# Performance work log

Measured on AMD Instinct MI355X. Metric: run time of the kernel, lower is better.

Reference implementation:

```python
import jax, jax.numpy as jnp
import numpy as np

SIGMA = 0.248
PRNUM = 6
P = 7.5
K = 3.0
ALPHA = 2.5


def _gauss_kernel():
    # 5x5 normalized Gaussian, replicated per channel for depthwise conv [O=3,I=1,5,5]
    x = jnp.arange(-2, 3, dtype=jnp.float32)
    x2, y2 = jnp.meshgrid(x, x, indexing='xy')
    k = jnp.exp(-(x2 ** 2 + y2 ** 2) / (2.0 * SIGMA ** 2))
    k = k / jnp.sum(k)
    return jnp.broadcast_to(k[None, None], (3, 1, 5, 5))


def _dwconv(x, k):
    # x: [3,H,W]; depthwise 5x5 conv, padding=2 (matches F.conv2d(..., padding=2, groups=3))
    return jax.lax.conv_general_dilated(
        x[None], k, window_strides=(1, 1), padding=[(2, 2), (2, 2)],
        feature_group_count=3, dimension_numbers=('NCHW', 'OIHW', 'NCHW'))[0]


def _down2(x):
    # torch bilinear align_corners=False at exact scale 0.5 == 2x2 average pooling
    c, h, w = x.shape
    return x.reshape(c, h // 2, 2, w // 2, 2).mean(axis=(2, 4))


def _up(x, hw):
    # torch bilinear align_corners=False upsample (half-pixel centers) == jax linear resize
    return jax.image.resize(x, (x.shape[0], hw[0], hw[1]), method='linear')


def _foveate(img, fixs):
    C, H, W = img.shape
    k = _gauss_kernel()
    # build Gaussian pyramid
    G = img
    pyr = [G]
    for _ in range(1, PRNUM):
        G = _down2(_dwconv(G, k))
        pyr.append(G)
    # re-expand each level back to full res (interpolate then blur at each step)
    As = [pyr[0]]
    for i in range(1, PRNUM):
        cur = pyr[i]
        for j in range(i):
            hw = (cur.shape[1] * 2, cur.shape[2] * 2) if j < i - 1 else (H, W)
            cur = _dwconv(_up(cur, hw), k)
        As.append(cur)
    As = jnp.stack(As)  # [prNum, 3, H, W]

    # radial eccentricity map (min distance over fixations)
    x = jnp.arange(W, dtype=jnp.float32)
    y = jnp.arange(H, dtype=jnp.float32)
    x2d, y2d = jnp.meshgrid(x, y, indexing='xy')  # each [H, W]
    d = jnp.sqrt((x2d[None] - fixs[:, 0, None, None]) ** 2 +
                 (y2d[None] - fixs[:, 1, None, None]) ** 2) / P
    theta = jnp.min(d, axis=0)
    R = ALPHA / (theta + ALPHA)

    Ts = [jnp.exp(-((2.0 ** (i - 3)) * R / SIGMA) ** 2 * K) for i in range(1, PRNUM)]
    Ts.append(jnp.zeros_like(R))

    om = np.minimum(np.sqrt(np.log(2.0) / K) / (2.0 ** np.arange(-2, 3)) * SIGMA, 1.0)
    omega = np.concatenate([om, [0.0]]).astype(np.float32)  # [prNum]

    layer_ind = jnp.zeros_like(R)
    for i in range(1, PRNUM):
        ind = (R >= omega[i]) & (R <= omega[i - 1])
        layer_ind = jnp.where(ind, jnp.float32(i), layer_ind)

    Bs = [(0.5 - Ts[i]) / (Ts[i - 1] - Ts[i] + 1e-5) for i in range(1, PRNUM)]

    Ms = []
    for i in range(PRNUM):
        base = jnp.ones_like(R) if i == 0 else 1.0 - Bs[i - 1]
        M = jnp.where(layer_ind == i, base, jnp.float32(0.0))
        if i < PRNUM - 1:
            M = jnp.where(layer_ind == i + 1, Bs[i], M)
        Ms.append(M)
    Ms = jnp.stack(Ms)  # [prNum, H, W]

    # blend: sum_p Ms[p] * As[p, c]
    im_fov = jnp.einsum('phw,pchw->chw', Ms, As)
    return im_fov


def setup_inputs() -> dict:
    key = jax.random.key(0)
    k1, k2 = jax.random.split(key)
    img = jax.random.uniform(k1, (3, 2048, 2048), dtype=jnp.float32) * 255.0
    fixs = jax.random.uniform(k2, (4, 2), dtype=jnp.float32) * 2048.0
    return {'img': img, 'fixs': fixs}


def reference(img, fixs):
    return _foveate(img, fixs)
```

## Files before the change

kernel.cpp:

```cpp
#include <hip/hip_runtime.h>
#include <math.h>

#define HW2048 (2048ull*2048ull)
typedef float f4 __attribute__((ext_vector_type(4)));
typedef float f2 __attribute__((ext_vector_type(2)));

struct BP {
  float P[4][3];
  float D2[5];
  float cc[5];
};

__global__ __launch_bounds__(256) void down12_k(const float* __restrict__ img,
                                                float* __restrict__ C1,
                                                float* __restrict__ p2) {
  int X = blockIdx.x * 16 + threadIdx.x;
  int Y = blockIdx.y * 16 + threadIdx.y;
  int c = blockIdx.z;
  const float* ip = img + (size_t)c * HW2048 + (size_t)(4 * Y) * 2048 + 4 * X;
  f4 r0 = __builtin_nontemporal_load((const f4*)(ip));
  f4 r1 = __builtin_nontemporal_load((const f4*)(ip + 2048));
  f4 r2 = __builtin_nontemporal_load((const f4*)(ip + 4096));
  f4 r3 = __builtin_nontemporal_load((const f4*)(ip + 6144));
  float a00 = 0.25f * (r0.x + r0.y + r1.x + r1.y);
  float a01 = 0.25f * (r0.z + r0.w + r1.z + r1.w);
  float a10 = 0.25f * (r2.x + r2.y + r3.x + r3.y);
  float a11 = 0.25f * (r2.z + r2.w + r3.z + r3.w);
  float* cp = C1 + (size_t)c * 1048576 + (size_t)(2 * Y) * 1024 + 2 * X;
  f2 u; u.x = a00; u.y = a01; *(f2*)cp = u;
  f2 v; v.x = a10; v.y = a11; *(f2*)(cp + 1024) = v;
  p2[((size_t)c * 512 + Y) * 512 + X] = 0.25f * (a00 + a01 + a10 + a11);
}

__global__ __launch_bounds__(256) void down345_k(const float* __restrict__ p2,
                                                 float* __restrict__ p3,
                                                 float* __restrict__ p4,
                                                 float* __restrict__ p5) {
  __shared__ float t4[16][17];
  int tx = threadIdx.x, ty = threadIdx.y;
  int X = blockIdx.x * 16 + tx;
  int Y = blockIdx.y * 16 + ty;
  int c = blockIdx.z;
  const float* ip = p2 + (size_t)c * 262144 + (size_t)(4 * Y) * 512 + 4 * X;
  f4 r0 = *(const f4*)(ip);
  f4 r1 = *(const f4*)(ip + 512);
  f4 r2 = *(const f4*)(ip + 1024);
  f4 r3 = *(const f4*)(ip + 1536);
  float a00 = 0.25f * (r0.x + r0.y + r1.x + r1.y);
  float a01 = 0.25f * (r0.z + r0.w + r1.z + r1.w);
  float a10 = 0.25f * (r2.x + r2.y + r3.x + r3.y);
  float a11 = 0.25f * (r2.z + r2.w + r3.z + r3.w);
  float* cp = p3 + (size_t)c * 65536 + (size_t)(2 * Y) * 256 + 2 * X;
  f2 u; u.x = a00; u.y = a01; *(f2*)cp = u;
  f2 v; v.x = a10; v.y = a11; *(f2*)(cp + 256) = v;
  float m = 0.25f * (a00 + a01 + a10 + a11);
  t4[ty][tx] = m;
  p4[((size_t)c * 128 + Y) * 128 + X] = m;
  __syncthreads();
  int tid = ty * 16 + tx;
  if (tid < 64) {
    int y = tid >> 3, x = tid & 7;
    float w = 0.25f * (t4[2*y][2*x] + t4[2*y][2*x+1] + t4[2*y+1][2*x] + t4[2*y+1][2*x+1]);
    p5[((size_t)c * 64 + blockIdx.y * 8 + y) * 64 + blockIdx.x * 8 + x] = w;
  }
}

__device__ __forceinline__ void up_coords(int o, int n, int& i0, int& i1, float& w0) {
  int m = o >> 1;
  if (o & 1) { i0 = m; i1 = min(m + 1, n - 1); w0 = 0.75f; }
  else       { i0 = max(m - 1, 0); i1 = m;     w0 = 0.25f; }
}

__global__ __launch_bounds__(256) void upchain_k(const float* __restrict__ p3,
                                                 const float* __restrict__ p4,
                                                 const float* __restrict__ p5,
                                                 float* __restrict__ U3,
                                                 float* __restrict__ U4,
                                                 float* __restrict__ U5) {
  __shared__ float a[19][20];
  __shared__ float mid[34][35];
  int z = blockIdx.z, im = z / 3, ch = z - im * 3;
  int X0 = blockIdx.x * 64, Y0 = blockIdx.y * 64;
  int tid = threadIdx.x;
  int bx1 = X0 / 4 - 1, by1 = Y0 / 4 - 1;
  int bx2 = X0 / 2 - 1, by2 = Y0 / 2 - 1;

  if (im == 2) {
    const float* s = p5 + ch * 4096;
    for (int j = tid; j < 18 * 18; j += 256) {
      int r = j / 18, cc = j % 18;
      int gy = min(max(by1 + r, 0), 127), gx = min(max(bx1 + cc, 0), 127);
      int r0, r1, c0, c1; float wy0, wx0;
      up_coords(gy, 64, r0, r1, wy0);
      up_coords(gx, 64, c0, c1, wx0);
      float wy1 = 1.f - wy0, wx1 = 1.f - wx0;
      a[r][cc] = wy0 * (wx0 * s[r0*64+c0] + wx1 * s[r0*64+c1])
               + wy1 * (wx0 * s[r1*64+c0] + wx1 * s[r1*64+c1]);
    }
    __syncthreads();
    for (int j = tid; j < 34 * 34; j += 256) {
      int r = j / 34, cc = j % 34;
      int gy = min(max(by2 + r, 0), 255), gx = min(max(bx2 + cc, 0), 255);
      int r0, r1, c0, c1; float wy0, wx0;
      up_coords(gy, 128, r0, r1, wy0);
      up_coords(gx, 128, c0, c1, wx0);
      float wy1 = 1.f - wy0, wx1 = 1.f - wx0;
      int a0 = r0 - by1, a1 = r1 - by1, b0 = c0 - bx1, b1 = c1 - bx1;
      mid[r][cc] = wy0 * (wx0 * a[a0][b0] + wx1 * a[a0][b1])
                 + wy1 * (wx0 * a[a1][b0] + wx1 * a[a1][b1]);
    }
    __syncthreads();
  } else if (im == 1) {
    const float* s = p4 + ch * 16384;
    for (int j = tid; j < 34 * 34; j += 256) {
      int r = j / 34, cc = j % 34;
      int gy = min(max(by2 + r, 0), 255), gx = min(max(bx2 + cc, 0), 255);
      int r0, r1, c0, c1; float wy0, wx0;
      up_coords(gy, 128, r0, r1, wy0);
      up_coords(gx, 128, c0, c1, wx0);
      float wy1 = 1.f - wy0, wx1 = 1.f - wx0;
      mid[r][cc] = wy0 * (wx0 * s[r0*128+c0] + wx1 * s[r0*128+c1])
                 + wy1 * (wx0 * s[r1*128+c0] + wx1 * s[r1*128+c1]);
    }
    __syncthreads();
  }

  float* dst = (im == 0) ? U3 : (im == 1) ? U4 : U5;
  const float* p3g = p3 + ch * 65536;
  int lx = tid & 63, lyb = tid >> 6;
#pragma unroll 4
  for (int rr = 0; rr < 16; ++rr) {
    int ly = lyb * 16 + rr;
    int x = X0 + lx, y = Y0 + ly;
    int r0, r1, c0, c1; float wy0, wx0;
    up_coords(y, 256, r0, r1, wy0);
    up_coords(x, 256, c0, c1, wx0);
    float wy1 = 1.f - wy0, wx1 = 1.f - wx0;
    float v;
    if (im == 0) {
      v = wy0 * (wx0 * p3g[r0*256+c0] + wx1 * p3g[r0*256+c1])
        + wy1 * (wx0 * p3g[r1*256+c0] + wx1 * p3g[r1*256+c1]);
    } else {
      int a0 = r0 - by2, a1 = r1 - by2, b0 = c0 - bx2, b1 = c1 - bx2;
      v = wy0 * (wx0 * mid[a0][b0] + wx1 * mid[a0][b1])
        + wy1 * (wx0 * mid[a1][b0] + wx1 * mid[a1][b1]);
    }
    dst[((size_t)ch * 512 + y) * 512 + x] = v;
  }
}

__device__ __forceinline__ void s2c(const float* __restrict__ b, int x0, int y0,
                                    const BP& bp, float o[2][4]) {
  int t = x0 >> 2, ky = y0 >> 2, yph = y0 & 3;
  int c[3], r[3];
#pragma unroll
  for (int j = 0; j < 3; ++j) {
    c[j] = min(max(t - 1 + j, 0), 511);
    r[j] = min(max(ky - 1 + j, 0), 511);
  }
  float v[3][3];
#pragma unroll
  for (int j = 0; j < 3; ++j) {
    const float* row = b + r[j] * 512;
    v[j][0] = row[c[0]]; v[j][1] = row[c[1]]; v[j][2] = row[c[2]];
  }
  const float* wr0 = bp.P[yph];
  const float* wr1 = bp.P[yph + 1];
  float rv0[3], rv1[3];
#pragma unroll
  for (int i = 0; i < 3; ++i) {
    rv0[i] = wr0[0] * v[0][i] + wr0[1] * v[1][i] + wr0[2] * v[2][i];
    rv1[i] = wr1[0] * v[0][i] + wr1[1] * v[1][i] + wr1[2] * v[2][i];
  }
#pragma unroll
  for (int p = 0; p < 4; ++p) {
    o[0][p] = bp.P[p][0] * rv0[0] + bp.P[p][1] * rv0[1] + bp.P[p][2] * rv0[2];
    o[1][p] = bp.P[p][0] * rv1[0] + bp.P[p][1] * rv1[1] + bp.P[p][2] * rv1[2];
  }
}

__device__ __forceinline__ void s1c(const float* __restrict__ b, int x0, int y0,
                                    float o[2][4]) {
  int q0 = x0 >> 1, qy = y0 >> 1;
  int c[4], r[3];
#pragma unroll
  for (int i = 0; i < 4; ++i) c[i] = min(max(q0 - 1 + i, 0), 1023);
#pragma unroll
  for (int j = 0; j < 3; ++j) r[j] = min(max(qy - 1 + j, 0), 1023);
  float v[3][4];
#pragma unroll
  for (int j = 0; j < 3; ++j) {
    const float* row = b + r[j] * 1024;
    v[j][0] = row[c[0]]; v[j][1] = row[c[1]]; v[j][2] = row[c[2]]; v[j][3] = row[c[3]];
  }
  float rv0[4], rv1[4];
#pragma unroll
  for (int i = 0; i < 4; ++i) {
    rv0[i] = 0.25f * v[0][i] + 0.75f * v[1][i];
    rv1[i] = 0.75f * v[1][i] + 0.25f * v[2][i];
  }
  o[0][0] = 0.25f * rv0[0] + 0.75f * rv0[1];
  o[0][1] = 0.75f * rv0[1] + 0.25f * rv0[2];
  o[0][2] = 0.25f * rv0[1] + 0.75f * rv0[2];
  o[0][3] = 0.75f * rv0[2] + 0.25f * rv0[3];
  o[1][0] = 0.25f * rv1[0] + 0.75f * rv1[1];
  o[1][1] = 0.75f * rv1[1] + 0.25f * rv1[2];
  o[1][2] = 0.25f * rv1[1] + 0.75f * rv1[2];
  o[1][3] = 0.75f * rv1[2] + 0.25f * rv1[3];
}

__device__ __forceinline__ void sample_level(int l, int x0, int y0,
    const float* __restrict__ imgc, const float* __restrict__ C1c,
    const float* __restrict__ b2, const float* __restrict__ b3,
    const float* __restrict__ b4, const float* __restrict__ b5,
    const BP& bp, float o[2][4]) {
  if (l == 0) {
    f4 v0 = *(const f4*)(imgc + (size_t)y0 * 2048 + x0);
    f4 v1 = *(const f4*)(imgc + (size_t)(y0 + 1) * 2048 + x0);
    o[0][0] = v0.x; o[0][1] = v0.y; o[0][2] = v0.z; o[0][3] = v0.w;
    o[1][0] = v1.x; o[1][1] = v1.y; o[1][2] = v1.z; o[1][3] = v1.w;
  } else if (l == 1) {
    s1c(C1c, x0, y0, o);
  } else {
    const float* b = (l == 2) ? b2 : (l == 3) ? b3 : (l == 4) ? b4 : b5;
    s2c(b, x0, y0, bp, o);
  }
}

__global__ __launch_bounds__(256) void fblend_k(
    const float* __restrict__ img, const float* __restrict__ C1,
    const float* __restrict__ B2, const float* __restrict__ B3,
    const float* __restrict__ B4, const float* __restrict__ B5,
    const float* __restrict__ fixs, int nf,
    float* __restrict__ out, BP bp) {
  int xs = blockIdx.x * 64 + threadIdx.x;
  int yp = blockIdx.y * 4 + threadIdx.y;
  int x0 = xs * 4, y0 = yp * 2;
  size_t ob0 = (size_t)y0 * 2048 + x0;

  float d2[2][4];
#pragma unroll
  for (int j = 0; j < 2; ++j)
#pragma unroll
    for (int i = 0; i < 4; ++i) d2[j][i] = 3.4e38f;
  for (int f = 0; f < nf; ++f) {
    float dx0 = (float)x0 - fixs[2 * f], dy0 = (float)y0 - fixs[2 * f + 1];
#pragma unroll
    for (int j = 0; j < 2; ++j) {
      float dy = dy0 + (float)j, dy2 = dy * dy;
#pragma unroll
      for (int i = 0; i < 4; ++i) {
        float dx = dx0 + (float)i;
        d2[j][i] = fminf(d2[j][i], dx * dx + dy2);
      }
    }
  }

  float dmn = d2[0][0], dmx = d2[0][0];
#pragma unroll
  for (int j = 0; j < 2; ++j)
#pragma unroll
    for (int i = 0; i < 4; ++i) {
      dmn = fminf(dmn, d2[j][i]);
      dmx = fmaxf(dmx, d2[j][i]);
    }
  int lmax = (dmx >= bp.D2[0]) + (dmx >= bp.D2[1]) + (dmx >= bp.D2[2]) +
             (dmx >= bp.D2[3]) + (dmx >= bp.D2[4]);

  if (lmax == 0) {
#pragma unroll
    for (int ch = 0; ch < 3; ++ch) {
      const float* imgc = img + (size_t)ch * HW2048;
      f4 v0 = *(const f4*)(imgc + ob0);
      f4 v1 = *(const f4*)(imgc + ob0 + 2048);
      __builtin_nontemporal_store(v0, (f4*)(out + (size_t)ch * HW2048 + ob0));
      __builtin_nontemporal_store(v1, (f4*)(out + (size_t)ch * HW2048 + ob0 + 2048));
    }
    return;
  }

  int lmin = (dmn >= bp.D2[0]) + (dmn >= bp.D2[1]) + (dmn >= bp.D2[2]) +
             (dmn >= bp.D2[3]) + (dmn >= bp.D2[4]);
  bool mixed = (lmin != lmax);

  float thr  = (lmax == 1) ? bp.D2[0] : (lmax == 2) ? bp.D2[1] :
               (lmax == 3) ? bp.D2[2] : (lmax == 4) ? bp.D2[3] : bp.D2[4];
  float cL_A = (lmax <= 4) ? ((lmax == 1) ? bp.cc[1] : (lmax == 2) ? bp.cc[2] :
               (lmax == 3) ? bp.cc[3] : bp.cc[4]) : bp.cc[4];
  float cm_A = (lmax == 1) ? bp.cc[0] : (lmax == 2) ? bp.cc[1] :
               (lmax == 3) ? bp.cc[2] : (lmax == 4) ? bp.cc[3] : bp.cc[4];
  float cL_B = cm_A;
  float cm_B = (lmax <= 2) ? bp.cc[0] : (lmax == 3) ? bp.cc[1] :
               (lmax == 4) ? bp.cc[2] : bp.cc[3];
  bool tsL_A_zero = (lmax >= 5);

  float Bv[2][4];
  bool  tp[2][4];
#pragma unroll
  for (int j = 0; j < 2; ++j)
#pragma unroll
    for (int i = 0; i < 4; ++i) {
      float dd = d2[j][i];
      bool top = (dd >= thr);
      tp[j][i] = top;
      float d = sqrtf(dd);
      float R = 18.75f / (d + 18.75f);
      float R2 = R * R;
      float cL = top ? cL_A : cL_B;
      float cm = top ? cm_A : cm_B;
      float tsL = (top && tsL_A_zero) ? 0.f : __expf(-cL * R2);
      float tsm = __expf(-cm * R2);
      float B = (0.5f - tsL) / (tsm - tsL + 1e-5f);
      if (!top && lmax == 1) B = 0.f;
      Bv[j][i] = B;
    }

#pragma unroll
  for (int ch = 0; ch < 3; ++ch) {
    const float* imgc = img + (size_t)ch * HW2048;
    const float* C1c  = C1 + (size_t)ch * 1048576;
    const float* b2   = B2 + (size_t)ch * 262144;
    const float* b3   = B3 + (size_t)ch * 262144;
    const float* b4   = B4 + (size_t)ch * 262144;
    const float* b5   = B5 + (size_t)ch * 262144;

    float sA[2][4];
    float sB[2][4];
    float sC[2][4];
    sample_level(lmax,     x0, y0, imgc, C1c, b2, b3, b4, b5, bp, sA);
    sample_level(lmax - 1, x0, y0, imgc, C1c, b2, b3, b4, b5, bp, sB);
#pragma unroll
    for (int j = 0; j < 2; ++j)
#pragma unroll
      for (int i = 0; i < 4; ++i) sC[j][i] = sB[j][i];
    if (mixed && lmax >= 2)
      sample_level(lmax - 2, x0, y0, imgc, C1c, b2, b3, b4, b5, bp, sC);

    float res[2][4];
#pragma unroll
    for (int j = 0; j < 2; ++j)
#pragma unroll
      for (int i = 0; i < 4; ++i) {
        float B = Bv[j][i];
        bool top = tp[j][i];
        float hi = top ? sA[j][i] : sB[j][i];
        float lo = top ? sB[j][i] : sC[j][i];
        res[j][i] = B * lo + (1.f - B) * hi;
      }

    f4 v0, v1;
    v0.x = res[0][0]; v0.y = res[0][1]; v0.z = res[0][2]; v0.w = res[0][3];
    v1.x = res[1][0]; v1.y = res[1][1]; v1.z = res[1][2]; v1.w = res[1][3];
    __builtin_nontemporal_store(v0, (f4*)(out + (size_t)ch * HW2048 + ob0));
    __builtin_nontemporal_store(v1, (f4*)(out + (size_t)ch * HW2048 + ob0 + 2048));
  }
}

extern "C" void kernel_launch(void* const* d_in, const int* in_sizes, int n_in,
                              void* d_out, int out_size, void* d_ws, size_t ws_size,
                              hipStream_t stream) {
  const float* img  = (const float*)d_in[0];
  const float* fixs = (const float*)d_in[1];
  int nf = in_sizes[1] / 2;
  float* out = (float*)d_out;
  float* ws  = (float*)d_ws;

  BP bp;
  const double sig = 0.248, Kd = 3.0, Pd = 7.5, Ad = 2.5;
  double obv = sqrt(log(2.0) / Kd) * sig;
  for (int j = 0; j < 5; ++j) {
    double om = obv * pow(2.0, 2 - j);
    double Dj = Pd * Ad * (1.0 / om - 1.0);
    bp.D2[j] = (float)(Dj * Dj);
  }
  for (int X = 0; X < 5; ++X)
    bp.cc[X] = (float)(Kd * pow(2.0, 2.0 * (X - 2)) / (sig * sig));
  const float Pt[4][3] = {{0.375f, 0.625f, 0.f},
                          {0.1875f, 0.75f, 0.0625f},
                          {0.0625f, 0.75f, 0.1875f},
                          {0.f, 0.625f, 0.375f}};
  for (int a = 0; a < 4; ++a) for (int t = 0; t < 3; ++t) bp.P[a][t] = Pt[a][t];

  size_t o = 0;
  float* C1 = ws + o; o += 3ull * 1024 * 1024;
  float* p2 = ws + o; o += 3ull * 512 * 512;
  float* p3 = ws + o; o += 3ull * 256 * 256;
  float* p4 = ws + o; o += 3ull * 128 * 128;
  float* p5 = ws + o; o += 3ull * 64 * 64;
  float* U3 = ws + o; o += 3ull * 512 * 512;
  float* U4 = ws + o; o += 3ull * 512 * 512;
  float* U5 = ws + o; o += 3ull * 512 * 512;

  down12_k  <<<dim3(32, 32, 3), dim3(16, 16), 0, stream>>>(img, C1, p2);
  down345_k <<<dim3(8, 8, 3),   dim3(16, 16), 0, stream>>>(p2, p3, p4, p5);
  upchain_k <<<dim3(8, 8, 9),   dim3(256),    0, stream>>>(p3, p4, p5, U3, U4, U5);
  fblend_k  <<<dim3(8, 256),    dim3(64, 4),  0, stream>>>(img, C1, p2, U3, U4, U5,
                                                           fixs, nf, out, bp);
}
```

Measured before the change: 134.9 us.

## Fuse pyramid downsampling kernels, widen upchain blocks, split blend across channels

Merges the two downsampling kernels into one that reduces all pyramid levels through shared memory, removing a launch and the re-read of level 2. The upsample kernel now uses 1024 threads per block with fewer rows per thread. The blend kernel assigns one channel per thread (768-thread blocks), so the per-pixel weight math is recomputed three times but more threads run in parallel. The coarse transition term is derived by squaring the existing exponential twice instead of calling a second exp. The fused downsample adds extra barriers, and most of its threads sit idle during the coarse reduction steps.

```diff
diff --git a/kernel.cpp b/kernel.cpp
--- a/kernel.cpp
+++ b/kernel.cpp
@@ -11,11 +11,18 @@
   float cc[5];
 };
 
-__global__ __launch_bounds__(256) void down12_k(const float* __restrict__ img,
-                                                float* __restrict__ C1,
-                                                float* __restrict__ p2) {
-  int X = blockIdx.x * 16 + threadIdx.x;
-  int Y = blockIdx.y * 16 + threadIdx.y;
+__global__ __launch_bounds__(256) void downAll_k(const float* __restrict__ img,
+                                                 float* __restrict__ C1,
+                                                 float* __restrict__ p2,
+                                                 float* __restrict__ p3,
+                                                 float* __restrict__ p4,
+                                                 float* __restrict__ p5) {
+  __shared__ float t2[16][17];
+  __shared__ float t3[8][9];
+  __shared__ float t4a[4][5];
+  int tx = threadIdx.x, ty = threadIdx.y;
+  int X = blockIdx.x * 16 + tx;
+  int Y = blockIdx.y * 16 + ty;
   int c = blockIdx.z;
   const float* ip = img + (size_t)c * HW2048 + (size_t)(4 * Y) * 2048 + 4 * X;
   f4 r0 = __builtin_nontemporal_load((const f4*)(ip));
@@ -29,39 +36,29 @@
   float* cp = C1 + (size_t)c * 1048576 + (size_t)(2 * Y) * 1024 + 2 * X;
   f2 u; u.x = a00; u.y = a01; *(f2*)cp = u;
   f2 v; v.x = a10; v.y = a11; *(f2*)(cp + 1024) = v;
-  p2[((size_t)c * 512 + Y) * 512 + X] = 0.25f * (a00 + a01 + a10 + a11);
-}
-
-__global__ __launch_bounds__(256) void down345_k(const float* __restrict__ p2,
-                                                 float* __restrict__ p3,
-                                                 float* __restrict__ p4,
-                                                 float* __restrict__ p5) {
-  __shared__ float t4[16][17];
-  int tx = threadIdx.x, ty = threadIdx.y;
-  int X = blockIdx.x * 16 + tx;
-  int Y = blockIdx.y * 16 + ty;
-  int c = blockIdx.z;
-  const float* ip = p2 + (size_t)c * 262144 + (size_t)(4 * Y) * 512 + 4 * X;
-  f4 r0 = *(const f4*)(ip);
-  f4 r1 = *(const f4*)(ip + 512);
-  f4 r2 = *(const f4*)(ip + 1024);
-  f4 r3 = *(const f4*)(ip + 1536);
-  float a00 = 0.25f * (r0.x + r0.y + r1.x + r1.y);
-  float a01 = 0.25f * (r0.z + r0.w + r1.z + r1.w);
-  float a10 = 0.25f * (r2.x + r2.y + r3.x + r3.y);
-  float a11 = 0.25f * (r2.z + r2.w + r3.z + r3.w);
-  float* cp = p3 + (size_t)c * 65536 + (size_t)(2 * Y) * 256 + 2 * X;
-  f2 u; u.x = a00; u.y = a01; *(f2*)cp = u;
-  f2 v; v.x = a10; v.y = a11; *(f2*)(cp + 256) = v;
   float m = 0.25f * (a00 + a01 + a10 + a11);
-  t4[ty][tx] = m;
-  p4[((size_t)c * 128 + Y) * 128 + X] = m;
+  p2[((size_t)c * 512 + Y) * 512 + X] = m;
+  t2[ty][tx] = m;
   __syncthreads();
   int tid = ty * 16 + tx;
   if (tid < 64) {
     int y = tid >> 3, x = tid & 7;
-    float w = 0.25f * (t4[2*y][2*x] + t4[2*y][2*x+1] + t4[2*y+1][2*x] + t4[2*y+1][2*x+1]);
-    p5[((size_t)c * 64 + blockIdx.y * 8 + y) * 64 + blockIdx.x * 8 + x] = w;
+    float w = 0.25f * (t2[2*y][2*x] + t2[2*y][2*x+1] + t2[2*y+1][2*x] + t2[2*y+1][2*x+1]);
+    p3[((size_t)c * 256 + blockIdx.y * 8 + y) * 256 + blockIdx.x * 8 + x] = w;
+    t3[y][x] = w;
+  }
+  __syncthreads();
+  if (tid < 16) {
+    int y = tid >> 2, x = tid & 3;
+    float w = 0.25f * (t3[2*y][2*x] + t3[2*y][2*x+1] + t3[2*y+1][2*x] + t3[2*y+1][2*x+1]);
+    p4[((size_t)c * 128 + blockIdx.y * 4 + y) * 128 + blockIdx.x * 4 + x] = w;
+    t4a[y][x] = w;
+  }
+  __syncthreads();
+  if (tid < 4) {
+    int y = tid >> 1, x = tid & 1;
+    float w = 0.25f * (t4a[2*y][2*x] + t4a[2*y][2*x+1] + t4a[2*y+1][2*x] + t4a[2*y+1][2*x+1]);
+    p5[((size_t)c * 64 + blockIdx.y * 2 + y) * 64 + blockIdx.x * 2 + x] = w;
   }
 }
 
@@ -71,12 +68,12 @@
   else       { i0 = max(m - 1, 0); i1 = m;     w0 = 0.25f; }
 }
 
-__global__ __launch_bounds__(256) void upchain_k(const float* __restrict__ p3,
-                                                 const float* __restrict__ p4,
-                                                 const float* __restrict__ p5,
-                                                 float* __restrict__ U3,
-                                                 float* __restrict__ U4,
-                                                 float* __restrict__ U5) {
+__global__ __launch_bounds__(1024) void upchain_k(const float* __restrict__ p3,
+                                                  const float* __restrict__ p4,
+                                                  const float* __restrict__ p5,
+                                                  float* __restrict__ U3,
+                                                  float* __restrict__ U4,
+                                                  float* __restrict__ U5) {
   __shared__ float a[19][20];
   __shared__ float mid[34][35];
   int z = blockIdx.z, im = z / 3, ch = z - im * 3;
@@ -87,7 +84,7 @@
 
   if (im == 2) {
     const float* s = p5 + ch * 4096;
-    for (int j = tid; j < 18 * 18; j += 256) {
+    for (int j = tid; j < 18 * 18; j += 1024) {
       int r = j / 18, cc = j % 18;
       int gy = min(max(by1 + r, 0), 127), gx = min(max(bx1 + cc, 0), 127);
       int r0, r1, c0, c1; float wy0, wx0;
@@ -98,7 +95,7 @@
                + wy1 * (wx0 * s[r1*64+c0] + wx1 * s[r1*64+c1]);
     }
     __syncthreads();
-    for (int j = tid; j < 34 * 34; j += 256) {
+    for (int j = tid; j < 34 * 34; j += 1024) {
       int r = j / 34, cc = j % 34;
       int gy = min(max(by2 + r, 0), 255), gx = min(max(bx2 + cc, 0), 255);
       int r0, r1, c0, c1; float wy0, wx0;
@@ -112,7 +109,7 @@
     __syncthreads();
   } else if (im == 1) {
     const float* s = p4 + ch * 16384;
-    for (int j = tid; j < 34 * 34; j += 256) {
+    for (int j = tid; j < 34 * 34; j += 1024) {
       int r = j / 34, cc = j % 34;
       int gy = min(max(by2 + r, 0), 255), gx = min(max(bx2 + cc, 0), 255);
       int r0, r1, c0, c1; float wy0, wx0;
@@ -128,9 +125,9 @@
   float* dst = (im == 0) ? U3 : (im == 1) ? U4 : U5;
   const float* p3g = p3 + ch * 65536;
   int lx = tid & 63, lyb = tid >> 6;
-#pragma unroll 4
-  for (int rr = 0; rr < 16; ++rr) {
-    int ly = lyb * 16 + rr;
+#pragma unroll
+  for (int rr = 0; rr < 4; ++rr) {
+    int ly = lyb * 4 + rr;
     int x = X0 + lx, y = Y0 + ly;
     int r0, r1, c0, c1; float wy0, wx0;
     up_coords(y, 256, r0, r1, wy0);
@@ -227,16 +224,20 @@
   }
 }
 
-__global__ __launch_bounds__(256) void fblend_k(
+__global__ __launch_bounds__(768) void fblend_k(
     const float* __restrict__ img, const float* __restrict__ C1,
     const float* __restrict__ B2, const float* __restrict__ B3,
     const float* __restrict__ B4, const float* __restrict__ B5,
     const float* __restrict__ fixs, int nf,
     float* __restrict__ out, BP bp) {
   int xs = blockIdx.x * 64 + threadIdx.x;
-  int yp = blockIdx.y * 4 + threadIdx.y;
+  int ty = threadIdx.y;
+  int ch = ty % 3;
+  int yp = blockIdx.y * 4 + (ty / 3);
   int x0 = xs * 4, y0 = yp * 2;
   size_t ob0 = (size_t)y0 * 2048 + x0;
+  const float* imgc = img + (size_t)ch * HW2048;
+  float* outc = out + (size_t)ch * HW2048;
 
   float d2[2][4];
 #pragma unroll
@@ -268,14 +269,10 @@
              (dmx >= bp.D2[3]) + (dmx >= bp.D2[4]);
 
   if (lmax == 0) {
-#pragma unroll
-    for (int ch = 0; ch < 3; ++ch) {
-      const float* imgc = img + (size_t)ch * HW2048;
-      f4 v0 = *(const f4*)(imgc + ob0);
-      f4 v1 = *(const f4*)(imgc + ob0 + 2048);
-      __builtin_nontemporal_store(v0, (f4*)(out + (size_t)ch * HW2048 + ob0));
-      __builtin_nontemporal_store(v1, (f4*)(out + (size_t)ch * HW2048 + ob0 + 2048));
-    }
+    f4 v0 = *(const f4*)(imgc + ob0);
+    f4 v1 = *(const f4*)(imgc + ob0 + 2048);
+    __builtin_nontemporal_store(v0, (f4*)(outc + ob0));
+    __builtin_nontemporal_store(v1, (f4*)(outc + ob0 + 2048));
     return;
   }
 
@@ -285,14 +282,11 @@
 
   float thr  = (lmax == 1) ? bp.D2[0] : (lmax == 2) ? bp.D2[1] :
                (lmax == 3) ? bp.D2[2] : (lmax == 4) ? bp.D2[3] : bp.D2[4];
-  float cL_A = (lmax <= 4) ? ((lmax == 1) ? bp.cc[1] : (lmax == 2) ? bp.cc[2] :
-               (lmax == 3) ? bp.cc[3] : bp.cc[4]) : bp.cc[4];
   float cm_A = (lmax == 1) ? bp.cc[0] : (lmax == 2) ? bp.cc[1] :
                (lmax == 3) ? bp.cc[2] : (lmax == 4) ? bp.cc[3] : bp.cc[4];
-  float cL_B = cm_A;
   float cm_B = (lmax <= 2) ? bp.cc[0] : (lmax == 3) ? bp.cc[1] :
                (lmax == 4) ? bp.cc[2] : bp.cc[3];
-  bool tsL_A_zero = (lmax >= 5);
+  bool top5 = (lmax >= 5);
 
   float Bv[2][4];
   bool  tp[2][4];
@@ -306,54 +300,50 @@
       float d = sqrtf(dd);
       float R = 18.75f / (d + 18.75f);
       float R2 = R * R;
-      float cL = top ? cL_A : cL_B;
       float cm = top ? cm_A : cm_B;
-      float tsL = (top && tsL_A_zero) ? 0.f : __expf(-cL * R2);
       float tsm = __expf(-cm * R2);
+      float t2 = tsm * tsm;
+      float tsL = (top && top5) ? 0.f : t2 * t2;
       float B = (0.5f - tsL) / (tsm - tsL + 1e-5f);
       if (!top && lmax == 1) B = 0.f;
       Bv[j][i] = B;
     }
 
-#pragma unroll
-  for (int ch = 0; ch < 3; ++ch) {
-    const float* imgc = img + (size_t)ch * HW2048;
-    const float* C1c  = C1 + (size_t)ch * 1048576;
-    const float* b2   = B2 + (size_t)ch * 262144;
-    const float* b3   = B3 + (size_t)ch * 262144;
-    const float* b4   = B4 + (size_t)ch * 262144;
-    const float* b5   = B5 + (size_t)ch * 262144;
-
-    float sA[2][4];
-    float sB[2][4];
-    float sC[2][4];
-    sample_level(lmax,     x0, y0, imgc, C1c, b2, b3, b4, b5, bp, sA);
-    sample_level(lmax - 1, x0, y0, imgc, C1c, b2, b3, b4, b5, bp, sB);
-#pragma unroll
-    for (int j = 0; j < 2; ++j)
-#pragma unroll
-      for (int i = 0; i < 4; ++i) sC[j][i] = sB[j][i];
-    if (mixed && lmax >= 2)
-      sample_level(lmax - 2, x0, y0, imgc, C1c, b2, b3, b4, b5, bp, sC);
-
-    float res[2][4];
-#pragma unroll
-    for (int j = 0; j < 2; ++j)
-#pragma unroll
-      for (int i = 0; i < 4; ++i) {
-        float B = Bv[j][i];
-        bool top = tp[j][i];
-        float hi = top ? sA[j][i] : sB[j][i];
-        float lo = top ? sB[j][i] : sC[j][i];
-        res[j][i] = B * lo + (1.f - B) * hi;
-      }
-
-    f4 v0, v1;
-    v0.x = res[0][0]; v0.y = res[0][1]; v0.z = res[0][2]; v0.w = res[0][3];
-    v1.x = res[1][0]; v1.y = res[1][1]; v1.z = res[1][2]; v1.w = res[1][3];
-    __builtin_nontemporal_store(v0, (f4*)(out + (size_t)ch * HW2048 + ob0));
-    __builtin_nontemporal_store(v1, (f4*)(out + (size_t)ch * HW2048 + ob0 + 2048));
-  }
+  const float* C1c = C1 + (size_t)ch * 1048576;
+  const float* b2  = B2 + (size_t)ch * 262144;
+  const float* b3  = B3 + (size_t)ch * 262144;
+  const float* b4  = B4 + (size_t)ch * 262144;
+  const float* b5  = B5 + (size_t)ch * 262144;
+
+  float sA[2][4];
+  float sB[2][4];
+  float sC[2][4];
+  sample_level(lmax,     x0, y0, imgc, C1c, b2, b3, b4, b5, bp, sA);
+  sample_level(lmax - 1, x0, y0, imgc, C1c, b2, b3, b4, b5, bp, sB);
+#pragma unroll
+  for (int j = 0; j < 2; ++j)
+#pragma unroll
+    for (int i = 0; i < 4; ++i) sC[j][i] = sB[j][i];
+  if (mixed && lmax >= 2)
+    sample_level(lmax - 2, x0, y0, imgc, C1c, b2, b3, b4, b5, bp, sC);
+
+  float res[2][4];
+#pragma unroll
+  for (int j = 0; j < 2; ++j)
+#pragma unroll
+    for (int i = 0; i < 4; ++i) {
+      float B = Bv[j][i];
+      bool top = tp[j][i];
+      float hi = top ? sA[j][i] : sB[j][i];
+      float lo = top ? sB[j][i] : sC[j][i];
+      res[j][i] = B * lo + (1.f - B) * hi;
+    }
+
+  f4 v0, v1;
+  v0.x = res[0][0]; v0.y = res[0][1]; v0.z = res[0][2]; v0.w = res[0][3];
+  v1.x = res[1][0]; v1.y = res[1][1]; v1.z = res[1][2]; v1.w = res[1][3];
+  __builtin_nontemporal_store(v0, (f4*)(outc + ob0));
+  __builtin_nontemporal_store(v1, (f4*)(outc + ob0 + 2048));
 }
 
 extern "C" void kernel_launch(void* const* d_in, const int* in_sizes, int n_in,
@@ -391,9 +381,8 @@
   float* U4 = ws + o; o += 3ull * 512 * 512;
   float* U5 = ws + o; o += 3ull * 512 * 512;
 
-  down12_k  <<<dim3(32, 32, 3), dim3(16, 16), 0, stream>>>(img, C1, p2);
-  down345_k <<<dim3(8, 8, 3),   dim3(16, 16), 0, stream>>>(p2, p3, p4, p5);
-  upchain_k <<<dim3(8, 8, 9),   dim3(256),    0, stream>>>(p3, p4, p5, U3, U4, U5);
-  fblend_k  <<<dim3(8, 256),    dim3(64, 4),  0, stream>>>(img, C1, p2, U3, U4, U5,
+  downAll_k <<<dim3(32, 32, 3), dim3(16, 16), 0, stream>>>(img, C1, p2, p3, p4, p5);
+  upchain_k <<<dim3(8, 8, 9),   dim3(1024),   0, stream>>>(p3, p4, p5, U3, U4, U5);
+  fblend_k  <<<dim3(8, 256),    dim3(64, 12), 0, stream>>>(img, C1, p2, U3, U4, U5,
                                                            fixs, nf, out, bp);
 }
```

Result: slower. 141.3 us (+4.8%).
